# Optimization experiments

Hardware: AMD Instinct MI355X
Metric: run time of the kernel (lower is better)

The kernel has to match this reference:

```python
import jax, jax.numpy as jnp
import numpy as np

B, T, N = 16, 512, 128
D, HID, S, H, L, EMB = 256, 128, 16, 512, 4, 512
EPS_BN = 1e-5
EPS_LN = 1e-5


def _ln(x, w, b):
    mu = x.mean(-1, keepdims=True)
    v = ((x - mu) ** 2).mean(-1, keepdims=True)
    return (x - mu) * jax.lax.rsqrt(v + EPS_LN) * w + b


def _bn(x, w, b):
    # x: (M, N, C); training-mode BatchNorm1d over (batch, spatial), biased var
    mu = x.mean((0, 1))
    v = x.var((0, 1))
    return (x - mu) * jax.lax.rsqrt(v + EPS_BN) * w + b


def setup_inputs() -> dict:
    key = jax.random.key(0)
    ks = iter(jax.random.split(key, 40))
    r = lambda *s: jax.random.normal(next(ks), s, jnp.float32) * 0.05
    inp = dict(
        x=jax.random.normal(next(ks), (B, T, N, 3), jnp.float32),
        lengths=jax.random.randint(next(ks), (B,), 0, T),
        conv1_w=r(HID, 3), bn1_w=1.0 + r(HID), bn1_b=r(HID),
        conv2_w=r(HID, HID), bn2_w=1.0 + r(HID), bn2_b=r(HID),
        fproj_w=r(D, HID), fproj_b=r(D),
        pre_ln_w=1.0 + r(D), pre_ln_b=r(D),
        in_w=r(L, 2 * H, D), in_b=r(L, 2 * H),
        conv_w=r(L, H, 1, 4), conv_b=r(L, H),
        A=r(L, H, S), Bm=r(L, H, S),
        out_w=r(L, D, H), out_b=r(L, D),
        post_ln_w=1.0 + r(D), post_ln_b=r(D),
        m1_w=r(1024, D), m1_b=r(1024),
        m2_w=r(1024, 1024), m2_b=r(1024),
        m3_w=r(EMB, 1024), m3_b=r(EMB),
    )
    return inp


def reference(x, lengths, conv1_w, bn1_w, bn1_b, conv2_w, bn2_w, bn2_b,
              fproj_w, fproj_b, pre_ln_w, pre_ln_b,
              in_w, in_b, conv_w, conv_b, A, Bm, out_w, out_b,
              post_ln_w, post_ln_b, m1_w, m1_b, m2_w, m2_b, m3_w, m3_b):
    Bb, Tt, Nn, _ = x.shape
    xf = x.reshape(Bb * Tt, Nn, 3)
    mu = xf.mean(1, keepdims=True)
    sd = jnp.std(xf, axis=1, ddof=1, keepdims=True) + 1e-10  # torch.std unbiased
    xn = (xf - mu) / sd

    # PointNet frame encoder (1x1 convs == per-point matmuls)
    h1 = jax.nn.relu(_bn(xn @ conv1_w.T, bn1_w, bn1_b))      # (BT, N, HID)
    h2 = jax.nn.relu(_bn(h1 @ conv2_w.T, bn2_w, bn2_b))
    feat = h2.max(1) @ fproj_w.T + fproj_b                   # (BT, D)

    seq = _ln(feat.reshape(Bb, Tt, D), pre_ln_w, pre_ln_b)
    mask = (jnp.arange(Tt)[None, :] < lengths[:, None]).astype(seq.dtype)  # (B, T)
    mk = mask[:, :, None]

    def mamba(seq, iw, ib, cw, cb, Ai, Bi, ow, ob):
        inp = seq @ iw.T + ib                                # (B, T, 2H)
        Hh = inp.shape[-1] // 2
        gate = jax.nn.sigmoid(inp[..., :Hh])
        upd = jax.nn.silu(inp[..., Hh:])
        u = jax.lax.conv_general_dilated(
            upd.transpose(0, 2, 1), cw, (1,), [(2, 2)],
            feature_group_count=Hh, dimension_numbers=('NCH', 'OIH', 'NCH'))
        u = (u + cb[:, None])[:, :, :seq.shape[1]].transpose(0, 2, 1)  # drop extra step
        # masked linear state scan == masked cumulative sum
        Bu = jnp.einsum('bth,hs->bts', u, Bi) * mk           # (B, T, S)
        hstate = jnp.cumsum(Bu, axis=1)
        out = jnp.einsum('bts,hs->bth', hstate, Ai) * gate * mk
        return out @ ow.T + ob

    for i in range(L):
        seq = mamba(seq, in_w[i], in_b[i], conv_w[i], conv_b[i], A[i], Bm[i], out_w[i], out_b[i])

    seq = _ln(seq, post_ln_w, post_ln_b)
    denom = jnp.maximum(lengths, 1).astype(seq.dtype)[:, None]
    pooled = (seq * mk).sum(1) / denom

    e = jax.nn.gelu(pooled @ m1_w.T + m1_b, approximate=False)
    e = jax.nn.gelu(e @ m2_w.T + m2_b, approximate=False)
    e = e @ m3_w.T + m3_b
    return e / jnp.maximum(jnp.linalg.norm(e, axis=1, keepdims=True), 1e-12)
```

## Files before the change

kernel.cpp:

```cpp
#include <hip/hip_runtime.h>
#include <hip/hip_bf16.h>
#include <math.h>

#define NFRM 8192
#define NPT  128
#define CH   128
#define DD   256
#define HH   512
#define SS   16
#define NL   4

typedef __attribute__((ext_vector_type(8))) short bf16x8;
typedef __attribute__((ext_vector_type(4))) float f32x4;
typedef unsigned short u16;

#define MFMA16 __builtin_amdgcn_mfma_f32_16x16x32_bf16


__device__ __forceinline__ float red256(float v, int tid, volatile float* sc) {
#pragma unroll
  for (int off = 32; off; off >>= 1) v += __shfl_down(v, off);
  __syncthreads();
  if ((tid & 63) == 0) sc[tid >> 6] = v;
  __syncthreads();
  return sc[0] + sc[1] + sc[2] + sc[3];
}

__device__ __forceinline__ float sigmoidf_(float x) { return 1.f / (1.f + __expf(-x)); }
__device__ __forceinline__ float geluf_(float x) { return 0.5f * x * (1.f + erff(x * 0.70710678118654752f)); }

__device__ __forceinline__ u16 f2bf(float f) {
  __hip_bfloat16 h = __float2bfloat16(f);
  return *(u16*)&h;
}
__device__ __forceinline__ float bf2f(u16 u) {
  union { unsigned int i; float f; } v; v.i = ((unsigned int)u) << 16; return v.f;
}


__global__ __launch_bounds__(256) void k_prep(const float* __restrict__ conv2_w,
    const float* __restrict__ fproj_w, const float* __restrict__ in_w, const float* __restrict__ out_w,
    const float* __restrict__ A, const float* __restrict__ Bm,
    const float* __restrict__ cw, const float* __restrict__ cb,
    u16* __restrict__ W2B, u16* __restrict__ fprojB, u16* __restrict__ inwB,
    u16* __restrict__ outwB, u16* __restrict__ albB, u16* __restrict__ BmTd,
    float* __restrict__ cbB) {
  int idx = blockIdx.x * 256 + threadIdx.x;
  if (idx < 16384) {
    int c = idx >> 7, k = idx & 127;
    int dst = c * 128 + ((((k >> 3) ^ (c & 7)) << 3) | (k & 7));
    W2B[dst] = f2bf(conv2_w[idx]);
    return;
  }
  idx -= 16384;
  if (idx < 32768) { fprojB[idx] = f2bf(fproj_w[idx]); return; }
  idx -= 32768;
  if (idx < 1048576) { inwB[idx] = f2bf(in_w[idx]); return; }
  idx -= 1048576;
  if (idx < 524288) { outwB[idx] = f2bf(out_w[idx]); return; }
  idx -= 524288;
  if (idx < 65536) {
    int l = idx >> 14, rem = idx & 16383, h = rem >> 5, kk = rem & 31;
    albB[idx] = (kk < 16) ? f2bf(A[(size_t)l * 8192 + h * 16 + kk]) : (u16)0;
    return;
  }
  idx -= 65536;
  if (idx < 131072) {
    int l = idx >> 15, rem = idx & 32767;
    int d = rem >> 13, rem2 = rem & 8191, s = rem2 >> 9, h = rem2 & 511;
    BmTd[idx] = f2bf(cw[(size_t)l * 2048 + h * 4 + d] * Bm[(size_t)l * 8192 + h * 16 + s]);
    return;
  }
  idx -= 131072;
  if (idx < 4096) {
    int wsl = idx >> 6, lane = idx & 63;
    int l = wsl >> 4, s = wsl & 15;
    float acc = 0.f;
    for (int h = lane; h < 512; h += 64)
      acc = fmaf(cb[l * 512 + h], Bm[(size_t)l * 8192 + h * 16 + s], acc);
#pragma unroll
    for (int off = 32; off; off >>= 1) acc += __shfl_down(acc, off);
    if (lane == 0) cbB[wsl] = acc;
  }
}

__global__ __launch_bounds__(256) void k_mom(const float* __restrict__ x, float* __restrict__ msd,
                                             float* __restrict__ pstat) {
  __shared__ float mpart[4][6];
  int tid = threadIdx.x, lane = tid & 63, w = tid >> 6;
  int f = blockIdx.x * 4 + w;
  const float* xf = x + (size_t)f * 384 + lane * 6;
  float a0 = xf[0], a1 = xf[1], a2 = xf[2], b0 = xf[3], b1 = xf[4], b2 = xf[5];
  float s0 = a0 + b0, s1 = a1 + b1, s2 = a2 + b2;
  float p00 = a0*a0 + b0*b0, p01 = a0*a1 + b0*b1, p02 = a0*a2 + b0*b2;
  float p11 = a1*a1 + b1*b1, p12 = a1*a2 + b1*b2, p22 = a2*a2 + b2*b2;
#pragma unroll
  for (int off = 32; off; off >>= 1) {
    s0 += __shfl_down(s0, off); s1 += __shfl_down(s1, off); s2 += __shfl_down(s2, off);
    p00 += __shfl_down(p00, off); p01 += __shfl_down(p01, off); p02 += __shfl_down(p02, off);
    p11 += __shfl_down(p11, off); p12 += __shfl_down(p12, off); p22 += __shfl_down(p22, off);
  }
  if (lane == 0) {
    float mu0 = s0 * (1.f/128.f), mu1 = s1 * (1.f/128.f), mu2 = s2 * (1.f/128.f);
    float C00 = p00 - 128.f*mu0*mu0, C01 = p01 - 128.f*mu0*mu1, C02 = p02 - 128.f*mu0*mu2;
    float C11 = p11 - 128.f*mu1*mu1, C12 = p12 - 128.f*mu1*mu2, C22 = p22 - 128.f*mu2*mu2;
    float sd0 = sqrtf(C00 * (1.f/127.f)) + 1e-10f;
    float sd1 = sqrtf(C11 * (1.f/127.f)) + 1e-10f;
    float sd2 = sqrtf(C22 * (1.f/127.f)) + 1e-10f;
    mpart[w][0] = C00/(sd0*sd0); mpart[w][1] = C01/(sd0*sd1); mpart[w][2] = C02/(sd0*sd2);
    mpart[w][3] = C11/(sd1*sd1); mpart[w][4] = C12/(sd1*sd2); mpart[w][5] = C22/(sd2*sd2);
    float* d = msd + (size_t)f * 8;
    d[0] = mu0; d[1] = mu1; d[2] = mu2; d[3] = 0.f;
    d[4] = 1.f/sd0; d[5] = 1.f/sd1; d[6] = 1.f/sd2; d[7] = 0.f;
  }
  __syncthreads();
  if (tid < 8) {
    float tot = 0.f;
    if (tid < 6) { for (int w2 = 0; w2 < 4; ++w2) tot += mpart[w2][tid]; }
    pstat[blockIdx.x * 8 + tid] = tot;
  }
}

__global__ __launch_bounds__(256) void k_stats2(const float* __restrict__ pstat, const float* __restrict__ w1,
    const float* __restrict__ bw, const float* __restrict__ bb, float* __restrict__ cc) {
  __shared__ float part[32][8];
  __shared__ float Mt[8];
  int tid = threadIdx.x, j = tid & 7, g = tid >> 3;
  float sm = 0.f;
  for (int r = g; r < 2048; r += 32) sm += pstat[r * 8 + j];
  part[g][j] = sm;
  __syncthreads();
  if (tid < 8) { float tot = 0.f; for (int g2 = 0; g2 < 32; ++g2) tot += part[g2][tid]; Mt[tid] = tot; }
  __syncthreads();
  if (tid < 128) {
    float w0 = w1[tid*3], wa = w1[tid*3+1], wb = w1[tid*3+2];
    float var = (w0*w0*Mt[0] + wa*wa*Mt[3] + wb*wb*Mt[5]
               + 2.f*(w0*wa*Mt[1] + w0*wb*Mt[2] + wa*wb*Mt[4])) * (1.f/1048576.f);
    float s = bw[tid] / sqrtf(var + 1e-5f);
    ((float4*)cc)[tid] = make_float4(s*w0, s*wa, s*wb, bb[tid]);
  }
}

__global__ __launch_bounds__(256) void k2_main(const float* __restrict__ x, const float4* __restrict__ cc,
    const float4* __restrict__ msd4, const u16* __restrict__ W2B,
    float* __restrict__ z2mx, float* __restrict__ z2mn,
    float* __restrict__ psum, float* __restrict__ psq) {
  __shared__ alignas(16) u16 w2s[16384];
  __shared__ float4 ccs[144];
  __shared__ float smx[4][CH], smn[4][CH], ssm[4][CH], ssq[4][CH];
  int tid = threadIdx.x;
  for (int i = tid; i < 2048; i += 256) ((float4*)w2s)[i] = ((const float4*)W2B)[i];
  if (tid < 128) ccs[tid + (tid >> 3)] = cc[tid];
  int lane = tid & 63, w = tid >> 6;
  int lr = lane & 15, kg = lane >> 4;
  int row0 = w * 32 + lr, row1 = row0 + 16;
  for (int fi = 0; fi < 8; ++fi) {
    int f = blockIdx.x * 8 + fi;
    __syncthreads();
    float4 mu4 = msd4[f * 2], rs4 = msd4[f * 2 + 1];
    const float* xr0 = x + (size_t)f * 384 + row0 * 3;
    const float* xr1 = x + (size_t)f * 384 + row1 * 3;
    float xa0 = (xr0[0] - mu4.x) * rs4.x, xa1 = (xr0[1] - mu4.y) * rs4.y, xa2 = (xr0[2] - mu4.z) * rs4.z;
    float xb0 = (xr1[0] - mu4.x) * rs4.x, xb1 = (xr1[1] - mu4.y) * rs4.y, xb2 = (xr1[2] - mu4.z) * rs4.z;
    f32x4 acc[2][8];
#pragma unroll
    for (int fr = 0; fr < 2; ++fr)
#pragma unroll
      for (int fc = 0; fc < 8; ++fc) acc[fr][fc] = (f32x4){0.f, 0.f, 0.f, 0.f};
#pragma unroll
    for (int ks = 0; ks < 4; ++ks) {
      int kc = ks * 4 + kg;
      int base9 = kc * 9;
      bf16x8 a0, a1;
#pragma unroll
      for (int q = 0; q < 8; ++q) {
        float4 c4 = ccs[base9 + q];
        float h0 = fmaxf(0.f, fmaf(xa0, c4.x, fmaf(xa1, c4.y, fmaf(xa2, c4.z, c4.w))));
        float h1 = fmaxf(0.f, fmaf(xb0, c4.x, fmaf(xb1, c4.y, fmaf(xb2, c4.z, c4.w))));
        a0[q] = (short)f2bf(h0); a1[q] = (short)f2bf(h1);
      }
#pragma unroll
      for (int fc = 0; fc < 8; ++fc) {
        int col = fc * 16 + lr;
        bf16x8 b = *(const bf16x8*)&w2s[col * 128 + ((kc ^ (col & 7)) << 3)];
        acc[0][fc] = MFMA16(a0, b, acc[0][fc], 0, 0, 0);
        acc[1][fc] = MFMA16(a1, b, acc[1][fc], 0, 0, 0);
      }
    }
#pragma unroll
    for (int fc = 0; fc < 8; ++fc) {
      float mx = -3e38f, mn = 3e38f, sm = 0.f, sq = 0.f;
#pragma unroll
      for (int fr = 0; fr < 2; ++fr)
#pragma unroll
        for (int r = 0; r < 4; ++r) {
          float v = acc[fr][fc][r];
          mx = fmaxf(mx, v); mn = fminf(mn, v); sm += v; sq = fmaf(v, v, sq);
        }
#pragma unroll
      for (int off = 16; off <= 32; off <<= 1) {
        mx = fmaxf(mx, __shfl_xor(mx, off));
        mn = fminf(mn, __shfl_xor(mn, off));
        sm += __shfl_xor(sm, off);
        sq += __shfl_xor(sq, off);
      }
      if (lane < 16) {
        int col = fc * 16 + lr;
        smx[w][col] = mx; smn[w][col] = mn; ssm[w][col] = sm; ssq[w][col] = sq;
      }
    }
    __syncthreads();
    if (tid < CH) {
      float mx = smx[0][tid], mn = smn[0][tid], sm = ssm[0][tid], sq = ssq[0][tid];
#pragma unroll
      for (int w2 = 1; w2 < 4; ++w2) {
        mx = fmaxf(mx, smx[w2][tid]); mn = fminf(mn, smn[w2][tid]);
        sm += ssm[w2][tid]; sq += ssq[w2][tid];
      }
      z2mx[(size_t)f * CH + tid] = mx;
      z2mn[(size_t)f * CH + tid] = mn;
      psum[(size_t)f * CH + tid] = sm;
      psq[(size_t)f * CH + tid]  = sq;
    }
  }
}

__global__ __launch_bounds__(256) void k_red1(const float* __restrict__ psum, const float* __restrict__ psq,
    float* __restrict__ prs, float* __restrict__ prq) {
  __shared__ float s0[2][128], s1[2][128];
  int tid = threadIdx.x, c = tid & 127, half = tid >> 7;
  int f0 = blockIdx.x * 128;
  float sm = 0.f, sq = 0.f;
  for (int fl = half; fl < 128; fl += 2) {
    size_t idx = (size_t)(f0 + fl) * 128 + c;
    sm += psum[idx]; sq += psq[idx];
  }
  s0[half][c] = sm; s1[half][c] = sq;
  __syncthreads();
  if (tid < 128) {
    prs[blockIdx.x * 128 + tid] = s0[0][tid] + s0[1][tid];
    prq[blockIdx.x * 128 + tid] = s1[0][tid] + s1[1][tid];
  }
}

__global__ __launch_bounds__(256) void k_red2(const float* __restrict__ prs, const float* __restrict__ prq,
    const float* __restrict__ w, const float* __restrict__ b, float* __restrict__ st,
    float invM, float eps) {
  __shared__ float s0[2][128], s1[2][128];
  int tid = threadIdx.x, c = tid & 127, half = tid >> 7;
  float sm = 0.f, sq = 0.f;
  for (int g = half; g < 64; g += 2) { sm += prs[g * 128 + c]; sq += prq[g * 128 + c]; }
  s0[half][c] = sm; s1[half][c] = sq;
  __syncthreads();
  if (tid < 128) {
    float tsm = s0[0][tid] + s0[1][tid], tsq = s1[0][tid] + s1[1][tid];
    float mean = tsm * invM;
    float var = tsq * invM - mean * mean;
    float s = w[tid] / sqrtf(var + eps);
    st[tid] = s;
    st[CH + tid] = b[tid] - mean * s;
  }
}

__global__ __launch_bounds__(512) void k_fi(const float* __restrict__ z2mx, const float* __restrict__ z2mn,
    const float* __restrict__ s2t2, const u16* __restrict__ fprojB, const float* __restrict__ fpb,
    const float* __restrict__ plw, const float* __restrict__ plb,
    const u16* __restrict__ inwB_l, const float* __restrict__ inb,
    u16* __restrict__ gate, u16* __restrict__ upd) {
  __shared__ alignas(16) u16 h2s[32 * 128];
  __shared__ float ft[32 * 260];
  __shared__ alignas(16) u16 as[32 * 256];
  int f0 = blockIdx.x * 32, tid = threadIdx.x;
  int lane = tid & 63, w = tid >> 6, lr = lane & 15, kg = lane >> 4;
  {
    int row = tid >> 4, cc = tid & 15, c0 = cc * 8;
    const float* zx = z2mx + (size_t)(f0 + row) * 128 + c0;
    const float* zn = z2mn + (size_t)(f0 + row) * 128 + c0;
    bf16x8 v;
#pragma unroll
    for (int q = 0; q < 8; ++q) {
      int c = c0 + q;
      float s = s2t2[c], t = s2t2[128 + c];
      float z = (s >= 0.f) ? zx[q] : zn[q];
      v[q] = (short)f2bf(fmaxf(0.f, fmaf(s, z, t)));
    }
    *(bf16x8*)&h2s[row * 128 + ((cc ^ (row & 7)) << 3)] = v;
  }
  __syncthreads();
  {
    f32x4 fac[2][2];
#pragma unroll
    for (int fr = 0; fr < 2; ++fr)
#pragma unroll
      for (int fc = 0; fc < 2; ++fc) fac[fr][fc] = (f32x4){0.f, 0.f, 0.f, 0.f};
#pragma unroll
    for (int ks = 0; ks < 4; ++ks) {
      int kc = ks * 4 + kg;
      bf16x8 a0 = *(const bf16x8*)&h2s[lr * 128 + ((kc ^ (lr & 7)) << 3)];
      bf16x8 a1 = *(const bf16x8*)&h2s[(16 + lr) * 128 + ((kc ^ (lr & 7)) << 3)];
#pragma unroll
      for (int fc = 0; fc < 2; ++fc) {
        int d = w * 32 + fc * 16 + lr;
        bf16x8 b = *(const bf16x8*)&fprojB[(size_t)d * 128 + kc * 8];
        fac[0][fc] = MFMA16(a0, b, fac[0][fc], 0, 0, 0);
        fac[1][fc] = MFMA16(a1, b, fac[1][fc], 0, 0, 0);
      }
    }
#pragma unroll
    for (int fr = 0; fr < 2; ++fr)
#pragma unroll
      for (int fc = 0; fc < 2; ++fc) {
        int d = w * 32 + fc * 16 + lr;
        float bias = fpb[d];
#pragma unroll
        for (int r = 0; r < 4; ++r) {
          int row = fr * 16 + kg * 4 + r;
          ft[row * 260 + d] = fac[fr][fc][r] + bias;
        }
      }
  }
  __syncthreads();
  {
    float4 plw4 = ((const float4*)plw)[lane];
    float4 plb4 = ((const float4*)plb)[lane];
#pragma unroll
    for (int q = 0; q < 4; ++q) {
      int row = w * 4 + q;
      float4 v = *(const float4*)&ft[row * 260 + lane * 4];
      float s = v.x + v.y + v.z + v.w;
#pragma unroll
      for (int off = 32; off; off >>= 1) s += __shfl_xor(s, off);
      float mu = s * (1.f / 256.f);
      float4 dd = make_float4(v.x - mu, v.y - mu, v.z - mu, v.w - mu);
      float qq = dd.x*dd.x + dd.y*dd.y + dd.z*dd.z + dd.w*dd.w;
#pragma unroll
      for (int off = 32; off; off >>= 1) qq += __shfl_xor(qq, off);
      float rs = 1.f / sqrtf(qq * (1.f / 256.f) + 1e-5f);
      u16 o[4];
      o[0] = f2bf(fmaf(dd.x * rs, plw4.x, plb4.x));
      o[1] = f2bf(fmaf(dd.y * rs, plw4.y, plb4.y));
      o[2] = f2bf(fmaf(dd.z * rs, plw4.z, plb4.z));
      o[3] = f2bf(fmaf(dd.w * rs, plw4.w, plb4.w));
      int chunk = lane >> 1;
      *(uint2*)&as[row * 256 + ((chunk ^ (row & 7)) << 3) + (lane & 1) * 4] = *(uint2*)o;
    }
  }
  __syncthreads();
  f32x4 acc[2][8];
#pragma unroll
  for (int fr = 0; fr < 2; ++fr)
#pragma unroll
    for (int fc = 0; fc < 8; ++fc) acc[fr][fc] = (f32x4){0.f, 0.f, 0.f, 0.f};
  int colb = w * 128;
#pragma unroll
  for (int ks = 0; ks < 8; ++ks) {
    int kc = ks * 4 + kg;
    int r1 = 16 + lr;
    bf16x8 a0 = *(const bf16x8*)&as[lr * 256 + ((kc ^ (lr & 7)) << 3)];
    bf16x8 a1 = *(const bf16x8*)&as[r1 * 256 + ((kc ^ (r1 & 7)) << 3)];
#pragma unroll
    for (int fc = 0; fc < 8; ++fc) {
      int col = colb + fc * 16 + lr;
      bf16x8 b = *(const bf16x8*)&inwB_l[(size_t)col * 256 + kc * 8];
      acc[0][fc] = MFMA16(a0, b, acc[0][fc], 0, 0, 0);
      acc[1][fc] = MFMA16(a1, b, acc[1][fc], 0, 0, 0);
    }
  }
  bool isGate = (w < 4);
  u16* dst = isGate ? gate : upd;
  int cbOff = isGate ? 0 : 512;
#pragma unroll
  for (int fr = 0; fr < 2; ++fr)
#pragma unroll
    for (int fc = 0; fc < 8; ++fc) {
      int cg = colb + fc * 16 + lr;
      float bias = inb[cg];
      int colOut = cg - cbOff;
#pragma unroll
      for (int r = 0; r < 4; ++r) {
        int frame = f0 + fr * 16 + kg * 4 + r;
        float v = acc[fr][fc][r] + bias;
        float sg = sigmoidf_(v);
        v = isGate ? sg : v * sg;
        dst[(size_t)frame * 512 + colOut] = f2bf(v);
      }
    }
}

__global__ __launch_bounds__(512) void k_bu(const u16* __restrict__ updB, const u16* __restrict__ BmTd_l,
    const float* __restrict__ cbB_l, const int* __restrict__ lengths, float* __restrict__ bu) {
  __shared__ float part[2][64][16];
  int tid = threadIdx.x, lane = tid & 63, w = tid >> 6;
  int wf = w & 3, hh = w >> 2;
  int f0 = blockIdx.x * 64 + wf * 16;
  int lr = lane & 15, kg = lane >> 4;
  int t = (f0 & 511) + lr;
  const u16* arow = updB + (size_t)(f0 + lr) * 512;
  bool v0 = (t >= 2), v1 = (t >= 1), v3 = (t <= 510);
  const bf16x8 zv = (bf16x8){0,0,0,0,0,0,0,0};
  f32x4 acc = (f32x4){0.f, 0.f, 0.f, 0.f};
#pragma unroll
  for (int ks = 0; ks < 8; ++ks) {
    int kc = hh * 32 + ks * 4 + kg, co = kc * 8;
    bf16x8 a0 = v0 ? *(const bf16x8*)&arow[co - 1024] : zv;
    bf16x8 a1 = v1 ? *(const bf16x8*)&arow[co - 512]  : zv;
    bf16x8 a2 =      *(const bf16x8*)&arow[co];
    bf16x8 a3 = v3 ? *(const bf16x8*)&arow[co + 512]  : zv;
    acc = MFMA16(a0, *(const bf16x8*)&BmTd_l[0 * 8192 + lr * 512 + co], acc, 0, 0, 0);
    acc = MFMA16(a1, *(const bf16x8*)&BmTd_l[1 * 8192 + lr * 512 + co], acc, 0, 0, 0);
    acc = MFMA16(a2, *(const bf16x8*)&BmTd_l[2 * 8192 + lr * 512 + co], acc, 0, 0, 0);
    acc = MFMA16(a3, *(const bf16x8*)&BmTd_l[3 * 8192 + lr * 512 + co], acc, 0, 0, 0);
  }
#pragma unroll
  for (int r = 0; r < 4; ++r) part[hh][wf * 16 + kg * 4 + r][lr] = acc[r];
  __syncthreads();
  int len = lengths[blockIdx.x >> 3];
  for (int i = tid; i < 1024; i += 512) {
    int fl = i >> 4, s = i & 15;
    int frame = blockIdx.x * 64 + fl;
    int tt = frame & 511, bi = frame >> 9;
    float val = part[0][fl][s] + part[1][fl][s] + cbB_l[s];
    bu[((size_t)bi * 16 + s) * 512 + tt] = (tt < len) ? val : 0.f;
  }
}

__global__ __launch_bounds__(512) void k_mo(const float* __restrict__ bu,
    u16* __restrict__ gateB, u16* __restrict__ updB,
    const u16* __restrict__ albB_l, const u16* __restrict__ outwB_l, const float* __restrict__ outb,
    const u16* __restrict__ inwB_n, const float* __restrict__ inb_n,
    const int* __restrict__ lengths) {
  __shared__ alignas(16) u16 hsb[32 * 40];
  __shared__ alignas(16) u16 vl[32 * 512];
  __shared__ alignas(16) u16 as[32 * 256];
  int f0 = blockIdx.x * 32, tid = threadIdx.x;
  int bb = f0 >> 9, tbase = f0 & 511;
  int len = lengths[bb];
  int lane = tid & 63, w = tid >> 6, lr = lane & 15, kg = lane >> 4;
  for (int i = tid; i < 640; i += 512) ((unsigned int*)hsb)[i] = 0;
  __syncthreads();
#pragma unroll
  for (int q = 0; q < 2; ++q) {
    int s = w * 2 + q;
    const float* src = bu + ((size_t)bb * 16 + s) * 512 + lane * 8;
    float4 v0 = *(const float4*)src, v1 = *(const float4*)(src + 4);
    float p0 = v0.x, p1 = p0 + v0.y, p2 = p1 + v0.z, p3 = p2 + v0.w;
    float p4 = p3 + v1.x, p5 = p4 + v1.y, p6 = p5 + v1.z, p7 = p6 + v1.w;
    float tot = p7;
#pragma unroll
    for (int off = 1; off < 64; off <<= 1) {
      float n = __shfl_up(tot, off);
      if (lane >= off) tot += n;
    }
    float excl = tot - p7;
    int rbase = lane * 8 - tbase;
    if (rbase >= 0 && rbase < 32) {
      hsb[(rbase + 0) * 40 + s] = f2bf(p0 + excl);
      hsb[(rbase + 1) * 40 + s] = f2bf(p1 + excl);
      hsb[(rbase + 2) * 40 + s] = f2bf(p2 + excl);
      hsb[(rbase + 3) * 40 + s] = f2bf(p3 + excl);
      hsb[(rbase + 4) * 40 + s] = f2bf(p4 + excl);
      hsb[(rbase + 5) * 40 + s] = f2bf(p5 + excl);
      hsb[(rbase + 6) * 40 + s] = f2bf(p6 + excl);
      hsb[(rbase + 7) * 40 + s] = f2bf(p7 + excl);
    }
  }
  __syncthreads();
  {
    bf16x8 a0 = *(const bf16x8*)&hsb[lr * 40 + kg * 8];
    bf16x8 a1 = *(const bf16x8*)&hsb[(16 + lr) * 40 + kg * 8];
    f32x4 zero = (f32x4){0.f, 0.f, 0.f, 0.f};
#pragma unroll
    for (int fc = 0; fc < 4; ++fc) {
      int h = w * 64 + fc * 16 + lr;
      bf16x8 b = *(const bf16x8*)&albB_l[h * 32 + kg * 8];
      f32x4 va = MFMA16(a0, b, zero, 0, 0, 0);
      f32x4 vb = MFMA16(a1, b, zero, 0, 0, 0);
      int hck = h >> 3, hlo = h & 7;
#pragma unroll
      for (int fr = 0; fr < 2; ++fr) {
        f32x4 vv = fr ? vb : va;
#pragma unroll
        for (int r = 0; r < 4; ++r) {
          int fl = fr * 16 + kg * 4 + r;
          int frame = f0 + fl;
          float g = bf2f(gateB[(size_t)frame * 512 + h]);
          float val = ((frame & 511) < len) ? vv[r] * g : 0.f;
          vl[fl * 512 + ((hck ^ (fl & 7)) << 3) + hlo] = f2bf(val);
        }
      }
    }
  }
  __syncthreads();
  {
    f32x4 acc2[2][2];
#pragma unroll
    for (int fr = 0; fr < 2; ++fr)
#pragma unroll
      for (int fc = 0; fc < 2; ++fc) acc2[fr][fc] = (f32x4){0.f, 0.f, 0.f, 0.f};
    int db = w * 32;
#pragma unroll
    for (int ks = 0; ks < 16; ++ks) {
      int kc = ks * 4 + kg;
      int r1 = 16 + lr;
      bf16x8 a0 = *(const bf16x8*)&vl[lr * 512 + ((kc ^ (lr & 7)) << 3)];
      bf16x8 a1 = *(const bf16x8*)&vl[r1 * 512 + ((kc ^ (r1 & 7)) << 3)];
#pragma unroll
      for (int fc = 0; fc < 2; ++fc) {
        int d = db + fc * 16 + lr;
        bf16x8 b = *(const bf16x8*)&outwB_l[(size_t)d * 512 + kc * 8];
        acc2[0][fc] = MFMA16(a0, b, acc2[0][fc], 0, 0, 0);
        acc2[1][fc] = MFMA16(a1, b, acc2[1][fc], 0, 0, 0);
      }
    }
#pragma unroll
    for (int fr = 0; fr < 2; ++fr)
#pragma unroll
      for (int fc = 0; fc < 2; ++fc) {
        int d = db + fc * 16 + lr;
        float bias = outb[d];
        int dck = d >> 3, dlo = d & 7;
#pragma unroll
        for (int r = 0; r < 4; ++r) {
          int row = fr * 16 + kg * 4 + r;
          as[row * 256 + ((dck ^ (row & 7)) << 3) + dlo] = f2bf(acc2[fr][fc][r] + bias);
        }
      }
  }
  __syncthreads();
  f32x4 acc[2][8];
#pragma unroll
  for (int fr = 0; fr < 2; ++fr)
#pragma unroll
    for (int fc = 0; fc < 8; ++fc) acc[fr][fc] = (f32x4){0.f, 0.f, 0.f, 0.f};
  int colb = w * 128;
#pragma unroll
  for (int ks = 0; ks < 8; ++ks) {
    int kc = ks * 4 + kg;
    int r1 = 16 + lr;
    bf16x8 a0 = *(const bf16x8*)&as[lr * 256 + ((kc ^ (lr & 7)) << 3)];
    bf16x8 a1 = *(const bf16x8*)&as[r1 * 256 + ((kc ^ (r1 & 7)) << 3)];
#pragma unroll
    for (int fc = 0; fc < 8; ++fc) {
      int col = colb + fc * 16 + lr;
      bf16x8 b = *(const bf16x8*)&inwB_n[(size_t)col * 256 + kc * 8];
      acc[0][fc] = MFMA16(a0, b, acc[0][fc], 0, 0, 0);
      acc[1][fc] = MFMA16(a1, b, acc[1][fc], 0, 0, 0);
    }
  }
  bool isGate = (w < 4);
  u16* dst = isGate ? gateB : updB;
  int cbOff = isGate ? 0 : 512;
#pragma unroll
  for (int fr = 0; fr < 2; ++fr)
#pragma unroll
    for (int fc = 0; fc < 8; ++fc) {
      int cg = colb + fc * 16 + lr;
      float bias = inb_n[cg];
      int colOut = cg - cbOff;
#pragma unroll
      for (int r = 0; r < 4; ++r) {
        int frame = f0 + fr * 16 + kg * 4 + r;
        float v = acc[fr][fc][r] + bias;
        float sg = sigmoidf_(v);
        v = isGate ? sg : v * sg;
        dst[(size_t)frame * 512 + colOut] = f2bf(v);
      }
    }
}

__global__ __launch_bounds__(256) void k_out(const float* __restrict__ bu, const u16* __restrict__ gateB,
    const u16* __restrict__ albB_l, const u16* __restrict__ outwB_l, const float* __restrict__ outb,
    const int* __restrict__ lengths, float* __restrict__ sout) {
  __shared__ alignas(16) u16 hsb[32 * 40];
  __shared__ alignas(16) u16 vl[32 * 512];
  int f0 = blockIdx.x * 32, tid = threadIdx.x;
  int bb = f0 >> 9, tbase = f0 & 511;
  int len = lengths[bb];
  int lane = tid & 63, w = tid >> 6, lr = lane & 15, kg = lane >> 4;
  for (int i = tid; i < 640; i += 256) ((unsigned int*)hsb)[i] = 0;
  __syncthreads();
#pragma unroll
  for (int q = 0; q < 4; ++q) {
    int s = w * 4 + q;
    const float* src = bu + ((size_t)bb * 16 + s) * 512 + lane * 8;
    float4 v0 = *(const float4*)src, v1 = *(const float4*)(src + 4);
    float p0 = v0.x, p1 = p0 + v0.y, p2 = p1 + v0.z, p3 = p2 + v0.w;
    float p4 = p3 + v1.x, p5 = p4 + v1.y, p6 = p5 + v1.z, p7 = p6 + v1.w;
    float tot = p7;
#pragma unroll
    for (int off = 1; off < 64; off <<= 1) {
      float n = __shfl_up(tot, off);
      if (lane >= off) tot += n;
    }
    float excl = tot - p7;
    int rbase = lane * 8 - tbase;
    if (rbase >= 0 && rbase < 32) {
      hsb[(rbase + 0) * 40 + s] = f2bf(p0 + excl);
      hsb[(rbase + 1) * 40 + s] = f2bf(p1 + excl);
      hsb[(rbase + 2) * 40 + s] = f2bf(p2 + excl);
      hsb[(rbase + 3) * 40 + s] = f2bf(p3 + excl);
      hsb[(rbase + 4) * 40 + s] = f2bf(p4 + excl);
      hsb[(rbase + 5) * 40 + s] = f2bf(p5 + excl);
      hsb[(rbase + 6) * 40 + s] = f2bf(p6 + excl);
      hsb[(rbase + 7) * 40 + s] = f2bf(p7 + excl);
    }
  }
  __syncthreads();
  {
    bf16x8 a0 = *(const bf16x8*)&hsb[lr * 40 + kg * 8];
    bf16x8 a1 = *(const bf16x8*)&hsb[(16 + lr) * 40 + kg * 8];
    f32x4 zero = (f32x4){0.f, 0.f, 0.f, 0.f};
#pragma unroll
    for (int fc = 0; fc < 8; ++fc) {
      int h = w * 128 + fc * 16 + lr;
      bf16x8 b = *(const bf16x8*)&albB_l[h * 32 + kg * 8];
      f32x4 va = MFMA16(a0, b, zero, 0, 0, 0);
      f32x4 vb = MFMA16(a1, b, zero, 0, 0, 0);
      int hck = h >> 3, hlo = h & 7;
#pragma unroll
      for (int fr = 0; fr < 2; ++fr) {
        f32x4 vv = fr ? vb : va;
#pragma unroll
        for (int r = 0; r < 4; ++r) {
          int fl = fr * 16 + kg * 4 + r;
          int frame = f0 + fl;
          float g = bf2f(gateB[(size_t)frame * 512 + h]);
          float val = ((frame & 511) < len) ? vv[r] * g : 0.f;
          vl[fl * 512 + ((hck ^ (fl & 7)) << 3) + hlo] = f2bf(val);
        }
      }
    }
  }
  __syncthreads();
  f32x4 acc[2][4];
#pragma unroll
  for (int fr = 0; fr < 2; ++fr)
#pragma unroll
    for (int fc = 0; fc < 4; ++fc) acc[fr][fc] = (f32x4){0.f, 0.f, 0.f, 0.f};
  int db = w * 64;
#pragma unroll
  for (int ks = 0; ks < 16; ++ks) {
    int kc = ks * 4 + kg;
    int r1 = 16 + lr;
    bf16x8 a0 = *(const bf16x8*)&vl[lr * 512 + ((kc ^ (lr & 7)) << 3)];
    bf16x8 a1 = *(const bf16x8*)&vl[r1 * 512 + ((kc ^ (r1 & 7)) << 3)];
#pragma unroll
    for (int fc = 0; fc < 4; ++fc) {
      int d = db + fc * 16 + lr;
      bf16x8 b = *(const bf16x8*)&outwB_l[(size_t)d * 512 + kc * 8];
      acc[0][fc] = MFMA16(a0, b, acc[0][fc], 0, 0, 0);
      acc[1][fc] = MFMA16(a1, b, acc[1][fc], 0, 0, 0);
    }
  }
#pragma unroll
  for (int fr = 0; fr < 2; ++fr)
#pragma unroll
    for (int fc = 0; fc < 4; ++fc) {
      int d = db + fc * 16 + lr;
      float bias = outb[d];
#pragma unroll
      for (int r = 0; r < 4; ++r) {
        int frame = f0 + fr * 16 + kg * 4 + r;
        sout[(size_t)frame * 256 + d] = acc[fr][fc][r] + bias;
      }
    }
}

__global__ __launch_bounds__(512) void k_pp(const float* __restrict__ seq, const int* __restrict__ lengths,
    const float* __restrict__ w, const float* __restrict__ b, float* __restrict__ pooled) {
  __shared__ float4 part[8][64];
  int bb = blockIdx.x, tid = threadIdx.x, lane = tid & 63, wv = tid >> 6;
  int len = lengths[bb];
  float4 w4 = ((const float4*)w)[lane], b4 = ((const float4*)b)[lane];
  float4 pacc = make_float4(0.f, 0.f, 0.f, 0.f);
  for (int it = 0; it < 64; ++it) {
    int t = it * 8 + wv;
    float4 v = ((const float4*)(seq + ((size_t)bb * 512 + t) * DD))[lane];
    float s = v.x + v.y + v.z + v.w;
#pragma unroll
    for (int off = 32; off; off >>= 1) s += __shfl_xor(s, off);
    float mu = s * (1.f / 256.f);
    float4 dd = make_float4(v.x - mu, v.y - mu, v.z - mu, v.w - mu);
    float q = dd.x*dd.x + dd.y*dd.y + dd.z*dd.z + dd.w*dd.w;
#pragma unroll
    for (int off = 32; off; off >>= 1) q += __shfl_xor(q, off);
    float rs = 1.f / sqrtf(q * (1.f / 256.f) + 1e-5f);
    if (t < len) {
      pacc.x += fmaf(dd.x * rs, w4.x, b4.x);
      pacc.y += fmaf(dd.y * rs, w4.y, b4.y);
      pacc.z += fmaf(dd.z * rs, w4.z, b4.z);
      pacc.w += fmaf(dd.w * rs, w4.w, b4.w);
    }
  }
  part[wv][lane] = pacc;
  __syncthreads();
  if (tid < 64) {
    float4 a = part[0][tid];
#pragma unroll
    for (int w2 = 1; w2 < 8; ++w2) {
      float4 p = part[w2][tid];
      a.x += p.x; a.y += p.y; a.z += p.z; a.w += p.w;
    }
    float inv = 1.f / (float)max(len, 1);
    ((float4*)(pooled + (size_t)bb * DD))[tid] = make_float4(a.x * inv, a.y * inv, a.z * inv, a.w * inv);
  }
}

__global__ __launch_bounds__(256) void k_mlp(const float* __restrict__ in, const float* __restrict__ W,
    const float* __restrict__ bias, float* __restrict__ out, int K, int Nout, int act) {
  __shared__ float lin[16 * 1024];
  int tid = threadIdx.x, lane = tid & 63, w = tid >> 6;
  for (int i = tid; i < 16 * K / 4; i += 256) ((float4*)lin)[i] = ((const float4*)in)[i];
  __syncthreads();
  int o = blockIdx.x * 4 + w;
  const float* wr = W + (size_t)o * K;
  float acc[16];
#pragma unroll
  for (int r = 0; r < 16; ++r) acc[r] = 0.f;
  for (int k = lane; k < K; k += 64) {
    float wv = wr[k];
#pragma unroll
    for (int r = 0; r < 16; ++r) acc[r] = fmaf(lin[r * K + k], wv, acc[r]);
  }
#pragma unroll
  for (int r = 0; r < 16; ++r) {
#pragma unroll
    for (int off = 32; off; off >>= 1) acc[r] += __shfl_xor(acc[r], off);
  }
  if (lane < 16) {
    float v = 0.f;
#pragma unroll
    for (int r = 0; r < 16; ++r) if (lane == r) v = acc[r];
    v += bias[o];
    if (act) v = geluf_(v);
    out[(size_t)lane * Nout + o] = v;
  }
}

__global__ __launch_bounds__(256) void k_norm(const float* __restrict__ e, float* __restrict__ out) {
  __shared__ float sc[4];
  int b = blockIdx.x, tid = threadIdx.x;
  float v0 = e[(size_t)b * 512 + tid], v1 = e[(size_t)b * 512 + 256 + tid];
  float ss = red256(v0 * v0 + v1 * v1, tid, sc);
  float nrm = fmaxf(sqrtf(ss), 1e-12f);
  out[(size_t)b * 512 + tid] = v0 / nrm;
  out[(size_t)b * 512 + 256 + tid] = v1 / nrm;
}


extern "C" void kernel_launch(void* const* d_in, const int* in_sizes, int n_in,
                              void* d_out, int out_size, void* d_ws, size_t ws_size,
                              hipStream_t stream) {
  const float* x         = (const float*)d_in[0];
  const int*   lengths   = (const int*)d_in[1];
  const float* conv1_w   = (const float*)d_in[2];
  const float* bn1_w     = (const float*)d_in[3];
  const float* bn1_b     = (const float*)d_in[4];
  const float* conv2_w   = (const float*)d_in[5];
  const float* bn2_w     = (const float*)d_in[6];
  const float* bn2_b     = (const float*)d_in[7];
  const float* fproj_w   = (const float*)d_in[8];
  const float* fproj_b   = (const float*)d_in[9];
  const float* pre_ln_w  = (const float*)d_in[10];
  const float* pre_ln_b  = (const float*)d_in[11];
  const float* in_w      = (const float*)d_in[12];
  const float* in_b      = (const float*)d_in[13];
  const float* conv_w    = (const float*)d_in[14];
  const float* conv_b    = (const float*)d_in[15];
  const float* A         = (const float*)d_in[16];
  const float* Bm        = (const float*)d_in[17];
  const float* out_w     = (const float*)d_in[18];
  const float* out_b     = (const float*)d_in[19];
  const float* post_ln_w = (const float*)d_in[20];
  const float* post_ln_b = (const float*)d_in[21];
  const float* m1_w      = (const float*)d_in[22];
  const float* m1_b      = (const float*)d_in[23];
  const float* m2_w      = (const float*)d_in[24];
  const float* m2_b      = (const float*)d_in[25];
  const float* m3_w      = (const float*)d_in[26];
  const float* m3_b      = (const float*)d_in[27];
  float* outp = (float*)d_out;

  float* wsf = (float*)d_ws;
  size_t o = 0;
  auto F32 = [&](size_t n) { float* p = wsf + o; o += (n + 63) & ~(size_t)63; return p; };
  float* psum   = F32(1048576);
  float* psq    = F32(1048576);
  float* z2mx   = F32(1048576);
  float* z2mn   = F32(1048576);
  float* msd    = F32(65536);
  float* pstat  = F32(16384);
  float* cc     = F32(512);
  float* s2t2   = F32(256);
  float* prs    = F32(8192);
  float* prq    = F32(8192);
  u16*   W2B    = (u16*)F32(8192);
  u16*   fprojB = (u16*)F32(16384);
  u16*   inwB   = (u16*)F32(524288);
  u16*   outwB  = (u16*)F32(262144);
  u16*   albB   = (u16*)F32(32768);
  u16*   BmTd   = (u16*)F32(65536);
  float* cbB    = F32(64);
  float* seqA   = F32(2097152);
  u16*   gateB  = (u16*)F32(2097152);
  u16*   updB   = (u16*)F32(2097152);
  float* buv    = F32(131072);
  float* pooled = F32(4096);
  float* e1     = F32(16384);
  float* e2     = F32(16384);
  float* e3     = F32(8192);
  if (ws_size < o * sizeof(float)) return;

  const float invM = 1.f / (float)(NFRM * NPT);

  k_prep<<<7120, 256, 0, stream>>>(conv2_w, fproj_w, in_w, out_w, A, Bm, conv_w, conv_b,
                                   W2B, fprojB, inwB, outwB, albB, BmTd, cbB);
  k_mom<<<2048, 256, 0, stream>>>(x, msd, pstat);
  k_stats2<<<1, 256, 0, stream>>>(pstat, conv1_w, bn1_w, bn1_b, cc);
  k2_main<<<NFRM / 8, 256, 0, stream>>>(x, (const float4*)cc, (const float4*)msd, W2B,
                                        z2mx, z2mn, psum, psq);
  k_red1<<<64, 256, 0, stream>>>(psum, psq, prs, prq);
  k_red2<<<1, 256, 0, stream>>>(prs, prq, bn2_w, bn2_b, s2t2, invM, 1e-5f);
  k_fi<<<NFRM / 32, 512, 0, stream>>>(z2mx, z2mn, s2t2, fprojB, fproj_b, pre_ln_w, pre_ln_b,
                                      inwB, in_b, gateB, updB);

  for (int l = 0; l < 3; ++l) {
    k_bu<<<NFRM / 64, 512, 0, stream>>>(updB, BmTd + (size_t)l * 32768, cbB + l * 16, lengths, buv);
    k_mo<<<NFRM / 32, 512, 0, stream>>>(buv, gateB, updB,
                                        albB + (size_t)l * 16384, outwB + (size_t)l * 131072,
                                        out_b + l * 256,
                                        inwB + (size_t)(l + 1) * 262144, in_b + (l + 1) * 1024,
                                        lengths);
  }
  k_bu<<<NFRM / 64, 512, 0, stream>>>(updB, BmTd + (size_t)3 * 32768, cbB + 3 * 16, lengths, buv);
  k_out<<<NFRM / 32, 256, 0, stream>>>(buv, gateB, albB + (size_t)3 * 16384,
                                       outwB + (size_t)3 * 131072, out_b + 3 * 256, lengths, seqA);
  k_pp<<<16, 512, 0, stream>>>(seqA, lengths, post_ln_w, post_ln_b, pooled);
  k_mlp<<<256, 256, 0, stream>>>(pooled, m1_w, m1_b, e1, 256, 1024, 1);
  k_mlp<<<256, 256, 0, stream>>>(e1, m2_w, m2_b, e2, 1024, 1024, 1);
  k_mlp<<<128, 256, 0, stream>>>(e2, m3_w, m3_b, e3, 1024, 512, 0);
  k_norm<<<16, 256, 0, stream>>>(e3, outp);
}
```

Measured before the change: 444.2 us.

## Vectorize weight conversion, prefetch next frame in k2_main, shrink k_bu blocks, vectorize MLP

Weight conversion in k_prep now handles four floats per thread through float4/ushort4 accesses, and its grid shrinks to match. k2_main loads the next frame's points and stats during the current frame's work and double-buffers the reduction shared arrays, so one barrier per frame can go. k_bu moves from 512-thread, 64-frame blocks to 256-thread, 32-frame blocks to put more blocks in flight. k_mlp reads weights and activations as float4. The changes are unrelated and mostly touch small or one-off kernels, so the overall effect is likely modest.

```diff
diff --git a/kernel.cpp b/kernel.cpp
--- a/kernel.cpp
+++ b/kernel.cpp
@@ -53,12 +53,27 @@
     return;
   }
   idx -= 16384;
-  if (idx < 32768) { fprojB[idx] = f2bf(fproj_w[idx]); return; }
-  idx -= 32768;
-  if (idx < 1048576) { inwB[idx] = f2bf(in_w[idx]); return; }
-  idx -= 1048576;
-  if (idx < 524288) { outwB[idx] = f2bf(out_w[idx]); return; }
-  idx -= 524288;
+  if (idx < 8192) {
+    float4 v = ((const float4*)fproj_w)[idx];
+    ushort4 o; o.x = f2bf(v.x); o.y = f2bf(v.y); o.z = f2bf(v.z); o.w = f2bf(v.w);
+    ((ushort4*)fprojB)[idx] = o;
+    return;
+  }
+  idx -= 8192;
+  if (idx < 262144) {
+    float4 v = ((const float4*)in_w)[idx];
+    ushort4 o; o.x = f2bf(v.x); o.y = f2bf(v.y); o.z = f2bf(v.z); o.w = f2bf(v.w);
+    ((ushort4*)inwB)[idx] = o;
+    return;
+  }
+  idx -= 262144;
+  if (idx < 131072) {
+    float4 v = ((const float4*)out_w)[idx];
+    ushort4 o; o.x = f2bf(v.x); o.y = f2bf(v.y); o.z = f2bf(v.z); o.w = f2bf(v.w);
+    ((ushort4*)outwB)[idx] = o;
+    return;
+  }
+  idx -= 131072;
   if (idx < 65536) {
     int l = idx >> 14, rem = idx & 16383, h = rem >> 5, kk = rem & 31;
     albB[idx] = (kk < 16) ? f2bf(A[(size_t)l * 8192 + h * 16 + kk]) : (u16)0;
@@ -147,21 +162,31 @@
     float* __restrict__ psum, float* __restrict__ psq) {
   __shared__ alignas(16) u16 w2s[16384];
   __shared__ float4 ccs[144];
-  __shared__ float smx[4][CH], smn[4][CH], ssm[4][CH], ssq[4][CH];
+  __shared__ float smx[2][4][CH], smn[2][4][CH], ssm[2][4][CH], ssq[2][4][CH];
   int tid = threadIdx.x;
   for (int i = tid; i < 2048; i += 256) ((float4*)w2s)[i] = ((const float4*)W2B)[i];
   if (tid < 128) ccs[tid + (tid >> 3)] = cc[tid];
   int lane = tid & 63, w = tid >> 6;
   int lr = lane & 15, kg = lane >> 4;
   int row0 = w * 32 + lr, row1 = row0 + 16;
+  int f0i = blockIdx.x * 8;
+  float4 mu4 = msd4[f0i * 2], rs4 = msd4[f0i * 2 + 1];
+  const float* xr0 = x + (size_t)f0i * 384 + row0 * 3;
+  const float* xr1 = x + (size_t)f0i * 384 + row1 * 3;
+  float cx0 = xr0[0], cx1 = xr0[1], cx2 = xr0[2];
+  float cx3 = xr1[0], cx4 = xr1[1], cx5 = xr1[2];
+  __syncthreads();
   for (int fi = 0; fi < 8; ++fi) {
     int f = blockIdx.x * 8 + fi;
-    __syncthreads();
-    float4 mu4 = msd4[f * 2], rs4 = msd4[f * 2 + 1];
-    const float* xr0 = x + (size_t)f * 384 + row0 * 3;
-    const float* xr1 = x + (size_t)f * 384 + row1 * 3;
-    float xa0 = (xr0[0] - mu4.x) * rs4.x, xa1 = (xr0[1] - mu4.y) * rs4.y, xa2 = (xr0[2] - mu4.z) * rs4.z;
-    float xb0 = (xr1[0] - mu4.x) * rs4.x, xb1 = (xr1[1] - mu4.y) * rs4.y, xb2 = (xr1[2] - mu4.z) * rs4.z;
+    int p = fi & 1;
+    float xa0 = (cx0 - mu4.x) * rs4.x, xa1 = (cx1 - mu4.y) * rs4.y, xa2 = (cx2 - mu4.z) * rs4.z;
+    float xb0 = (cx3 - mu4.x) * rs4.x, xb1 = (cx4 - mu4.y) * rs4.y, xb2 = (cx5 - mu4.z) * rs4.z;
+    int fn = (f + 1 < NFRM) ? f + 1 : f;
+    float4 nmu = msd4[fn * 2], nrs = msd4[fn * 2 + 1];
+    const float* nr0 = x + (size_t)fn * 384 + row0 * 3;
+    const float* nr1 = x + (size_t)fn * 384 + row1 * 3;
+    float nx0 = nr0[0], nx1 = nr0[1], nx2 = nr0[2];
+    float nx3 = nr1[0], nx4 = nr1[1], nx5 = nr1[2];
     f32x4 acc[2][8];
 #pragma unroll
     for (int fr = 0; fr < 2; ++fr)
@@ -206,22 +231,24 @@
       }
       if (lane < 16) {
         int col = fc * 16 + lr;
-        smx[w][col] = mx; smn[w][col] = mn; ssm[w][col] = sm; ssq[w][col] = sq;
+        smx[p][w][col] = mx; smn[p][w][col] = mn; ssm[p][w][col] = sm; ssq[p][w][col] = sq;
       }
     }
     __syncthreads();
     if (tid < CH) {
-      float mx = smx[0][tid], mn = smn[0][tid], sm = ssm[0][tid], sq = ssq[0][tid];
+      float mx = smx[p][0][tid], mn = smn[p][0][tid], sm = ssm[p][0][tid], sq = ssq[p][0][tid];
 #pragma unroll
       for (int w2 = 1; w2 < 4; ++w2) {
-        mx = fmaxf(mx, smx[w2][tid]); mn = fminf(mn, smn[w2][tid]);
-        sm += ssm[w2][tid]; sq += ssq[w2][tid];
+        mx = fmaxf(mx, smx[p][w2][tid]); mn = fminf(mn, smn[p][w2][tid]);
+        sm += ssm[p][w2][tid]; sq += ssq[p][w2][tid];
       }
       z2mx[(size_t)f * CH + tid] = mx;
       z2mn[(size_t)f * CH + tid] = mn;
       psum[(size_t)f * CH + tid] = sm;
       psq[(size_t)f * CH + tid]  = sq;
     }
+    cx0 = nx0; cx1 = nx1; cx2 = nx2; cx3 = nx3; cx4 = nx4; cx5 = nx5;
+    mu4 = nmu; rs4 = nrs;
   }
 }
 
@@ -387,12 +414,12 @@
     }
 }
 
-__global__ __launch_bounds__(512) void k_bu(const u16* __restrict__ updB, const u16* __restrict__ BmTd_l,
+__global__ __launch_bounds__(256) void k_bu(const u16* __restrict__ updB, const u16* __restrict__ BmTd_l,
     const float* __restrict__ cbB_l, const int* __restrict__ lengths, float* __restrict__ bu) {
-  __shared__ float part[2][64][16];
+  __shared__ float part[2][32][16];
   int tid = threadIdx.x, lane = tid & 63, w = tid >> 6;
-  int wf = w & 3, hh = w >> 2;
-  int f0 = blockIdx.x * 64 + wf * 16;
+  int wf = w & 1, hh = w >> 1;
+  int f0 = blockIdx.x * 32 + wf * 16;
   int lr = lane & 15, kg = lane >> 4;
   int t = (f0 & 511) + lr;
   const u16* arow = updB + (size_t)(f0 + lr) * 512;
@@ -414,10 +441,10 @@
 #pragma unroll
   for (int r = 0; r < 4; ++r) part[hh][wf * 16 + kg * 4 + r][lr] = acc[r];
   __syncthreads();
-  int len = lengths[blockIdx.x >> 3];
-  for (int i = tid; i < 1024; i += 512) {
+  int len = lengths[blockIdx.x >> 4];
+  for (int i = tid; i < 512; i += 256) {
     int fl = i >> 4, s = i & 15;
-    int frame = blockIdx.x * 64 + fl;
+    int frame = blockIdx.x * 32 + fl;
     int tt = frame & 511, bi = frame >> 9;
     float val = part[0][fl][s] + part[1][fl][s] + cbB_l[s];
     bu[((size_t)bi * 16 + s) * 512 + tt] = (tt < len) ? val : 0.f;
@@ -713,14 +740,18 @@
   for (int i = tid; i < 16 * K / 4; i += 256) ((float4*)lin)[i] = ((const float4*)in)[i];
   __syncthreads();
   int o = blockIdx.x * 4 + w;
-  const float* wr = W + (size_t)o * K;
+  const float4* wr4 = (const float4*)(W + (size_t)o * K);
   float acc[16];
 #pragma unroll
   for (int r = 0; r < 16; ++r) acc[r] = 0.f;
-  for (int k = lane; k < K; k += 64) {
-    float wv = wr[k];
-#pragma unroll
-    for (int r = 0; r < 16; ++r) acc[r] = fmaf(lin[r * K + k], wv, acc[r]);
+  for (int k4 = lane; k4 < K / 4; k4 += 64) {
+    float4 wv = wr4[k4];
+    int kb = k4 * 4;
+#pragma unroll
+    for (int r = 0; r < 16; ++r) {
+      float4 lv = *(const float4*)&lin[r * K + kb];
+      acc[r] = fmaf(lv.x, wv.x, fmaf(lv.y, wv.y, fmaf(lv.z, wv.z, fmaf(lv.w, wv.w, acc[r]))));
+    }
   }
 #pragma unroll
   for (int r = 0; r < 16; ++r) {
@@ -813,7 +844,7 @@
 
   const float invM = 1.f / (float)(NFRM * NPT);
 
-  k_prep<<<7120, 256, 0, stream>>>(conv2_w, fproj_w, in_w, out_w, A, Bm, conv_w, conv_b,
+  k_prep<<<2416, 256, 0, stream>>>(conv2_w, fproj_w, in_w, out_w, A, Bm, conv_w, conv_b,
                                    W2B, fprojB, inwB, outwB, albB, BmTd, cbB);
   k_mom<<<2048, 256, 0, stream>>>(x, msd, pstat);
   k_stats2<<<1, 256, 0, stream>>>(pstat, conv1_w, bn1_w, bn1_b, cc);
@@ -825,14 +856,14 @@
                                       inwB, in_b, gateB, updB);
 
   for (int l = 0; l < 3; ++l) {
-    k_bu<<<NFRM / 64, 512, 0, stream>>>(updB, BmTd + (size_t)l * 32768, cbB + l * 16, lengths, buv);
+    k_bu<<<NFRM / 32, 256, 0, stream>>>(updB, BmTd + (size_t)l * 32768, cbB + l * 16, lengths, buv);
     k_mo<<<NFRM / 32, 512, 0, stream>>>(buv, gateB, updB,
                                         albB + (size_t)l * 16384, outwB + (size_t)l * 131072,
                                         out_b + l * 256,
                                         inwB + (size_t)(l + 1) * 262144, in_b + (l + 1) * 1024,
                                         lengths);
   }
-  k_bu<<<NFRM / 64, 512, 0, stream>>>(updB, BmTd + (size_t)3 * 32768, cbB + 3 * 16, lengths, buv);
+  k_bu<<<NFRM / 32, 256, 0, stream>>>(updB, BmTd + (size_t)3 * 32768, cbB + 3 * 16, lengths, buv);
   k_out<<<NFRM / 32, 256, 0, stream>>>(buv, gateB, albB + (size_t)3 * 16384,
                                        outwB + (size_t)3 * 131072, out_b + 3 * 256, lengths, seqA);
   k_pp<<<16, 512, 0, stream>>>(seqA, lengths, post_ln_w, post_ln_b, pooled);
```

New measurement: 406.4 us. -8.5%, faster.
